# Performance work log

Hardware: AMD Instinct MI355X
Metric: run time of the kernel (lower is better)

Reference implementation:

```python
import jax, jax.numpy as jnp
import numpy as np

C = 64          # residual channels
N_LAYERS = 30
MAX_STEPS = 200
SQRT2 = 2.0 ** 0.5


def _conv1d(x, W, b, dilation=1, pad=0):
    # x: [B, Cin, T], W: [Cout, Cin, K], b: [Cout]
    y = jax.lax.conv_general_dilated(
        x, W, window_strides=(1,), padding=[(pad, pad)],
        rhs_dilation=(dilation,), dimension_numbers=('NCH', 'OIH', 'NCH'))
    return y + b[None, :, None]


def _silu(x):
    return x * jax.nn.sigmoid(x)


def _emb_table():
    steps = jnp.arange(MAX_STEPS, dtype=jnp.float32)[:, None]      # [200,1]
    dims = jnp.arange(64, dtype=jnp.float32)[None, :]              # [1,64]
    t = steps * 10.0 ** (dims * 4.0 / 63.0)                        # [200,64]
    return jnp.concatenate([jnp.sin(t), jnp.cos(t)], axis=1)       # [200,128]


def setup_inputs() -> dict:
    key = jax.random.key(0)
    ks = jax.random.split(key, 20)
    B, T = 4, 16384
    f32 = jnp.float32
    inp = {
        'audio': jax.random.normal(ks[0], (B, 1, T), dtype=f32),
        'diffusion_step': jax.random.randint(ks[1], (B,), 0, MAX_STEPS),
        # input projection Conv1d(1, 64, 1)
        'in_W': jax.random.normal(ks[2], (C, 1, 1), f32) * 1.0,
        'in_b': jax.random.normal(ks[3], (C,), f32) * 0.01,
        # diffusion embedding MLP 128->512->512
        'p1_W': jax.random.normal(ks[4], (512, 128), f32) * (1.0 / np.sqrt(128)),
        'p1_b': jnp.zeros((512,), f32),
        'p2_W': jax.random.normal(ks[5], (512, 512), f32) * (1.0 / np.sqrt(512)),
        'p2_b': jnp.zeros((512,), f32),
        # per-layer params (stacked over 30 layers)
        'dw_W': jax.random.normal(ks[6], (N_LAYERS, 2 * C, C, 3), f32) * (1.0 / np.sqrt(3 * C)),
        'dw_b': jnp.zeros((N_LAYERS, 2 * C), f32),
        'dp_W': jax.random.normal(ks[7], (N_LAYERS, C, 512), f32) * (1.0 / np.sqrt(512)),
        'dp_b': jnp.zeros((N_LAYERS, C), f32),
        'op_W': jax.random.normal(ks[8], (N_LAYERS, 2 * C, C, 1), f32) * (1.0 / np.sqrt(C)),
        'op_b': jnp.zeros((N_LAYERS, 2 * C), f32),
        # skip projection Conv1d(64,64,1)
        'sk_W': jax.random.normal(ks[9], (C, C, 1), f32) * (1.0 / np.sqrt(C)),
        'sk_b': jnp.zeros((C,), f32),
        # output projection Conv1d(64,1,1), weight zero-init like original
        'out_W': jnp.zeros((1, C, 1), f32),
        'out_b': jax.random.normal(ks[10], (1,), f32) * 0.01,
    }
    return inp


def reference(audio, diffusion_step, in_W, in_b, p1_W, p1_b, p2_W, p2_b,
              dw_W, dw_b, dp_W, dp_b, op_W, op_b, sk_W, sk_b, out_W, out_b):
    x = jax.nn.relu(_conv1d(audio, in_W, in_b))                    # [B,64,T]
    # diffusion embedding
    t = _emb_table()[diffusion_step]                               # [B,128]
    t = _silu(t @ p1_W.T + p1_b)                                   # [B,512]
    t = _silu(t @ p2_W.T + p2_b)                                   # [B,512]
    skip = None
    for i in range(N_LAYERS):
        d = 2 ** (i % 10)
        cond = (t @ dp_W[i].T + dp_b[i])[:, :, None]               # [B,64,1]
        y = _conv1d(x + cond, dw_W[i], dw_b[i], dilation=d, pad=d) # [B,128,T]
        gate, filt = y[:, :C], y[:, C:]
        y = jax.nn.sigmoid(gate) * jnp.tanh(filt)                  # [B,64,T]
        y = _conv1d(y, op_W[i], op_b[i])                           # [B,128,T]
        residual, sk = y[:, :C], y[:, C:]
        x = (x + residual) / SQRT2
        skip = sk if skip is None else skip + sk
    x = skip / np.sqrt(float(N_LAYERS)).astype(np.float32)
    x = jax.nn.relu(_conv1d(x, sk_W, sk_b))
    return _conv1d(x, out_W, out_b)                                # [B,1,T]
```

## Files before the change

### kernel.cpp

```cpp
#include <hip/hip_runtime.h>
#include <math.h>

#define C 64
#define NL 30
#define T 16384
#define B 4

typedef __bf16 bf16_t;
typedef __bf16 bf16x8 __attribute__((ext_vector_type(8)));
typedef __bf16 bf16x4 __attribute__((ext_vector_type(4)));
typedef float f32x4 __attribute__((ext_vector_type(4)));

typedef const __attribute__((address_space(1))) unsigned int glb_u32;
typedef __attribute__((address_space(3))) unsigned int lds_u32;

constexpr float INV_SQRT2   = 0.70710678118654752440f;
constexpr float INV_SQRT_NL = 0.18257418583505537115f;

__device__ __forceinline__ float fsig(float x) {
    return __builtin_amdgcn_rcpf(1.f + __builtin_amdgcn_exp2f(-1.44269504089f * x));
}
__device__ __forceinline__ float ftanh(float x) {
    return fmaf(2.f, __builtin_amdgcn_rcpf(1.f + __builtin_amdgcn_exp2f(-2.88539008178f * x)), -1.f);
}
__device__ __forceinline__ int swz(int off) { return off ^ ((off >> 3) & 0x70); }

__global__ void pack_weights(const float* __restrict__ dw_W,
                             const float* __restrict__ op_W,
                             const float* __restrict__ sk_W,
                             bf16_t* __restrict__ convpk,
                             bf16_t* __restrict__ oppk,
                             bf16_t* __restrict__ skpk) {
    int idx = blockIdx.x * 256 + threadIdx.x;
    const int ndw = NL * 128 * 192;
    const int nop = NL * 128 * 64;
    if (idx < ndw) {
        int k = idx % 192; int r = idx / 192;
        int oc = r % 128;  int l = r / 128;
        int tap = k >> 6, ic = k & 63;
        convpk[idx] = (bf16_t)dw_W[((l * 128 + oc) * 64 + ic) * 3 + tap];
    } else if (idx < ndw + nop) {
        oppk[idx - ndw] = (bf16_t)op_W[idx - ndw];
    } else if (idx < ndw + nop + 4096) {
        int j = idx - ndw - nop;
        skpk[j] = (bf16_t)(sk_W[j] * INV_SQRT_NL);
    }
}

__global__ void cond_embp1(const int* __restrict__ step,
                           const float* __restrict__ p1_W, const float* __restrict__ p1_b,
                           float* __restrict__ h1out) {
    __shared__ float e[128];
    __shared__ float red[256];
    int b = blockIdx.x, blk = blockIdx.y, tid = threadIdx.x;
    int s = step[b];
    if (tid < 128) {
        int d = tid & 63;
        float tf = (float)s * powf(10.f, (float)d * 4.f / 63.f);
        double td = (double)tf;
        e[tid] = (tid < 64) ? (float)sin(td) : (float)cos(td);
    }
    __syncthreads();
    int ol = tid >> 2, q = tid & 3;
    int o = blk * 64 + ol;
    const float4* wr = (const float4*)(p1_W + o * 128 + q * 32);
    const float4* ev = (const float4*)(e + q * 32);
    float a = 0.f;
    #pragma unroll
    for (int j = 0; j < 8; ++j) {
        float4 wv = wr[j]; float4 xv = ev[j];
        a = fmaf(wv.x, xv.x, a); a = fmaf(wv.y, xv.y, a);
        a = fmaf(wv.z, xv.z, a); a = fmaf(wv.w, xv.w, a);
    }
    red[tid] = a;
    __syncthreads();
    if (q == 0) {
        float v = red[tid] + red[tid + 1] + red[tid + 2] + red[tid + 3] + p1_b[o];
        h1out[b * 512 + o] = v / (1.f + expf(-v));
    }
}

__global__ void cond_p2(const float* __restrict__ h1,
                        const float* __restrict__ p2_W, const float* __restrict__ p2_b,
                        float* __restrict__ h2out) {
    __shared__ float red[256];
    int b = blockIdx.x, blk = blockIdx.y, tid = threadIdx.x;
    int ol = tid >> 2, q = tid & 3;
    int o = blk * 64 + ol;
    const float4* wr = (const float4*)(p2_W + o * 512 + q * 128);
    const float4* hv = (const float4*)(h1 + b * 512 + q * 128);
    float a = 0.f;
    #pragma unroll 8
    for (int j = 0; j < 32; ++j) {
        float4 wv = wr[j]; float4 xv = hv[j];
        a = fmaf(wv.x, xv.x, a); a = fmaf(wv.y, xv.y, a);
        a = fmaf(wv.z, xv.z, a); a = fmaf(wv.w, xv.w, a);
    }
    red[tid] = a;
    __syncthreads();
    if (q == 0) {
        float v = red[tid] + red[tid + 1] + red[tid + 2] + red[tid + 3] + p2_b[o];
        h2out[b * 512 + o] = v / (1.f + expf(-v));
    }
}

__global__ void cond_stage2(const float* __restrict__ h2,
                            const float* __restrict__ dp_W, const float* __restrict__ dp_b,
                            float* __restrict__ cond) {
    __shared__ float part[256];
    int l = blockIdx.x, b = blockIdx.y;
    int tid = threadIdx.x;
    int o = tid >> 2, q = tid & 3;
    const float4* wr = (const float4*)(dp_W + ((size_t)l * C + o) * 512 + q * 128);
    const float4* h = (const float4*)(h2 + b * 512 + q * 128);
    float a = 0.f;
    #pragma unroll 8
    for (int j = 0; j < 32; ++j) {
        float4 wv = wr[j]; float4 hv = h[j];
        a = fmaf(wv.x, hv.x, a); a = fmaf(wv.y, hv.y, a);
        a = fmaf(wv.z, hv.z, a); a = fmaf(wv.w, hv.w, a);
    }
    part[tid] = a;
    __syncthreads();
    if (q == 0) {
        cond[(l * B + b) * C + o] =
            part[tid] + part[tid + 1] + part[tid + 2] + part[tid + 3] + dp_b[l * C + o];
    }
}

__global__ void cond_fold(const bf16_t* __restrict__ convpk,
                          const float* __restrict__ dw_b,
                          const float* __restrict__ cond,
                          float* __restrict__ bias2) {
    int l = blockIdx.x, b = blockIdx.y;
    int oc = threadIdx.x;
    const bf16_t* wr = convpk + ((size_t)l * 128 + oc) * 192;
    const float* cd = cond + (l * B + b) * C;
    float a = dw_b[l * 128 + oc];
    #pragma unroll 3
    for (int tap = 0; tap < 3; ++tap) {
        #pragma unroll
        for (int ic = 0; ic < 64; ++ic)
            a = fmaf((float)wr[tap * 64 + ic], cd[ic], a);
    }
    bias2[(l * B + b) * 128 + oc] = a;
}

__global__ void in_conv(const float* __restrict__ audio,
                        const float* __restrict__ in_W, const float* __restrict__ in_b,
                        bf16_t* __restrict__ x) {
    int idx = blockIdx.x * 256 + threadIdx.x;
    int cb = idx & 7;
    int t = (idx >> 3) & (T - 1);
    int b = idx >> 17;
    float av = audio[b * T + t];
    bf16x8 o;
    #pragma unroll
    for (int j = 0; j < 8; ++j) {
        int c = cb * 8 + j;
        o[j] = (bf16_t)fmaxf(fmaf(in_W[c], av, in_b[c]), 0.f);
    }
    *(bf16x8*)(x + ((size_t)b * T + t) * 64 + cb * 8) = o;
}

__global__ __launch_bounds__(256) void layer_kernel(
    const bf16_t* __restrict__ x_in, bf16_t* __restrict__ x_out, bf16_t* __restrict__ skip,
    const bf16_t* __restrict__ convpk, const bf16_t* __restrict__ oppk,
    const float* __restrict__ bias2, const float* __restrict__ op_b,
    const bf16_t* __restrict__ zpage,
    int layer, int dil, int first)
{
    __shared__ uint4 smem_u[2048];
    char* sm = (char*)smem_u;

    int tid = threadIdx.x;
    int w = __builtin_amdgcn_readfirstlane(tid >> 6);
    int l = tid & 63;
    int lr = l & 15;
    int g = l >> 4;
    int b = blockIdx.y;
    int tbase = blockIdx.x * 128;
    const bf16_t* xb = x_in + (size_t)b * T * 64;

    bf16x8 cA[2][6];
    const bf16_t* cw = convpk + (size_t)layer * 128 * 192;
    #pragma unroll
    for (int mf = 0; mf < 2; ++mf)
        #pragma unroll
        for (int kf = 0; kf < 6; ++kf)
            cA[mf][kf] = *(const bf16x8*)(cw + (mf * 64 + w * 16 + lr) * 192 + kf * 32 + g * 8);
    bf16x8 oA[2][2];
    const bf16_t* ow = oppk + (size_t)layer * 128 * 64;
    #pragma unroll
    for (int mf = 0; mf < 2; ++mf)
        #pragma unroll
        for (int kf = 0; kf < 2; ++kf)
            oA[mf][kf] = *(const bf16x8*)(ow + (mf * 64 + w * 16 + lr) * 64 + kf * 32 + g * 8);

    f32x4 bC[2], bO[2];
    const float* b2 = bias2 + (layer * B + b) * 128;
    const float* ob = op_b + layer * 2 * C;
    #pragma unroll
    for (int mf = 0; mf < 2; ++mf)
        #pragma unroll
        for (int r = 0; r < 4; ++r) {
            bC[mf][r] = b2[mf * 64 + w * 16 + g * 4 + r];
            bO[mf][r] = ob[mf * 64 + w * 16 + g * 4 + r];
        }

    size_t bb = (size_t)b * T * 64;

    for (int st = 0; st < 2; ++st) {
        int t0 = tbase + st * 64;

        #pragma unroll
        for (int it = 0; it < 6; ++it) {
            int qq = it * 256 + w * 64 + l;
            int slice = qq >> 9;
            int row = (qq >> 3) & 63;
            int c16 = qq & 7;
            int ts = t0 + row + (slice - 1) * dil;
            int c16s = c16 ^ (row & 7);
            const bf16_t* src = ((unsigned)ts < (unsigned)T)
                ? (xb + (size_t)ts * 64 + c16s * 8)
                : (zpage + c16s * 8);
            __builtin_amdgcn_global_load_lds(
                (glb_u32*)src,
                (lds_u32*)(sm + (it * 256 + w * 64) * 16),
                16, 0, 0);
        }
        __syncthreads();

        f32x4 acc[2][4];
        #pragma unroll
        for (int mf = 0; mf < 2; ++mf)
            #pragma unroll
            for (int nf = 0; nf < 4; ++nf) acc[mf][nf] = bC[mf];
        #pragma unroll
        for (int kf = 0; kf < 6; ++kf) {
            int tap = kf >> 1;
            int kc = (kf & 1) * 32;
            bf16x8 Bf[4];
            #pragma unroll
            for (int nf = 0; nf < 4; ++nf) {
                int off = tap * 8192 + (nf * 16 + lr) * 128 + (kc + g * 8) * 2;
                Bf[nf] = *(const bf16x8*)(sm + swz(off));
            }
            #pragma unroll
            for (int mf = 0; mf < 2; ++mf)
                #pragma unroll
                for (int nf = 0; nf < 4; ++nf)
                    acc[mf][nf] = __builtin_amdgcn_mfma_f32_16x16x32_bf16(
                        cA[mf][kf], Bf[nf], acc[mf][nf], 0, 0, 0);
        }

        #pragma unroll
        for (int nf = 0; nf < 4; ++nf) {
            union { bf16_t h[4]; uint2 u; } zp;
            #pragma unroll
            for (int r = 0; r < 4; ++r)
                zp.h[r] = (bf16_t)(fsig(acc[0][nf][r]) * ftanh(acc[1][nf][r]));
            int off = 24576 + (nf * 16 + lr) * 128 + (w * 16 + g * 4) * 2;
            *(uint2*)(sm + swz(off)) = zp.u;
        }
        __syncthreads();

        f32x4 acc2[2][4];
        #pragma unroll
        for (int mf = 0; mf < 2; ++mf)
            #pragma unroll
            for (int nf = 0; nf < 4; ++nf) acc2[mf][nf] = bO[mf];
        #pragma unroll
        for (int kf = 0; kf < 2; ++kf) {
            bf16x8 Zf[4];
            #pragma unroll
            for (int nf = 0; nf < 4; ++nf) {
                int off = 24576 + (nf * 16 + lr) * 128 + (kf * 32 + g * 8) * 2;
                Zf[nf] = *(const bf16x8*)(sm + swz(off));
            }
            #pragma unroll
            for (int mf = 0; mf < 2; ++mf)
                #pragma unroll
                for (int nf = 0; nf < 4; ++nf)
                    acc2[mf][nf] = __builtin_amdgcn_mfma_f32_16x16x32_bf16(
                        oA[mf][kf], Zf[nf], acc2[mf][nf], 0, 0, 0);
        }

        #pragma unroll
        for (int nf = 0; nf < 4; ++nf) {
            int t = t0 + nf * 16 + lr;
            int c0 = w * 16 + g * 4;
            int xoff = 8192 + (nf * 16 + lr) * 128 + c0 * 2;
            bf16x4 xv = *(const bf16x4*)(sm + swz(xoff));
            bf16x4 ro, so;
            bf16_t* sp = skip + bb + (size_t)t * 64 + c0;
            if (first) {
                #pragma unroll
                for (int r = 0; r < 4; ++r) {
                    ro[r] = (bf16_t)(((float)xv[r] + acc2[0][nf][r]) * INV_SQRT2);
                    so[r] = (bf16_t)acc2[1][nf][r];
                }
            } else {
                bf16x4 sv = *(const bf16x4*)sp;
                #pragma unroll
                for (int r = 0; r < 4; ++r) {
                    ro[r] = (bf16_t)(((float)xv[r] + acc2[0][nf][r]) * INV_SQRT2);
                    so[r] = (bf16_t)((float)sv[r] + acc2[1][nf][r]);
                }
            }
            *(bf16x4*)(x_out + bb + (size_t)t * 64 + c0) = ro;
            *(bf16x4*)sp = so;
        }
        if (st == 0) __syncthreads();
    }
}

__global__ __launch_bounds__(256) void final_kernel(
    const bf16_t* __restrict__ skip, const bf16_t* __restrict__ skpk,
    const float* __restrict__ sk_b,
    const float* __restrict__ out_W, const float* __restrict__ out_b,
    float* __restrict__ out)
{
    __shared__ uint4 tile_u[512];
    __shared__ float part[16][66];
    unsigned char* sm = (unsigned char*)tile_u;
    int tid = threadIdx.x;
    int w = __builtin_amdgcn_readfirstlane(tid >> 6);
    int l = tid & 63, lr = l & 15, g = l >> 4;
    int b = blockIdx.y, t0 = blockIdx.x * 64;
    const bf16_t* sb = skip + (size_t)b * T * 64;

    #pragma unroll
    for (int it = 0; it < 2; ++it) {
        int q = it * 256 + tid;
        int row = q >> 3, c16 = q & 7;
        uint4 val = *(const uint4*)(sb + (size_t)(t0 + row) * 64 + c16 * 8);
        *(uint4*)(sm + swz(row * 128 + c16 * 16)) = val;
    }

    bf16x8 aS[2];
    #pragma unroll
    for (int kf = 0; kf < 2; ++kf)
        aS[kf] = *(const bf16x8*)(skpk + (w * 16 + lr) * 64 + kf * 32 + g * 8);
    f32x4 acc[4];
    #pragma unroll
    for (int nf = 0; nf < 4; ++nf)
        #pragma unroll
        for (int r = 0; r < 4; ++r) acc[nf][r] = sk_b[w * 16 + g * 4 + r];
    __syncthreads();

    #pragma unroll
    for (int kf = 0; kf < 2; ++kf) {
        bf16x8 Bf[4];
        #pragma unroll
        for (int nf = 0; nf < 4; ++nf) {
            int off = (nf * 16 + lr) * 128 + (kf * 32 + g * 8) * 2;
            Bf[nf] = *(const bf16x8*)(sm + swz(off));
        }
        #pragma unroll
        for (int nf = 0; nf < 4; ++nf)
            acc[nf] = __builtin_amdgcn_mfma_f32_16x16x32_bf16(aS[kf], Bf[nf], acc[nf], 0, 0, 0);
    }

    #pragma unroll
    for (int nf = 0; nf < 4; ++nf) {
        float o = 0.f;
        #pragma unroll
        for (int r = 0; r < 4; ++r)
            o = fmaf(out_W[w * 16 + g * 4 + r], fmaxf(acc[nf][r], 0.f), o);
        part[w * 4 + g][nf * 16 + lr] = o;
    }
    __syncthreads();
    if (tid < 64) {
        float o = out_b[0];
        #pragma unroll
        for (int j = 0; j < 16; ++j) o += part[j][tid];
        out[(size_t)b * T + t0 + tid] = o;
    }
}

extern "C" void kernel_launch(void* const* d_in, const int* in_sizes, int n_in,
                              void* d_out, int out_size, void* d_ws, size_t ws_size,
                              hipStream_t stream) {
    const float* audio = (const float*)d_in[0];
    const int*   dstep = (const int*)d_in[1];
    const float* in_W  = (const float*)d_in[2];
    const float* in_b  = (const float*)d_in[3];
    const float* p1_W  = (const float*)d_in[4];
    const float* p1_b  = (const float*)d_in[5];
    const float* p2_W  = (const float*)d_in[6];
    const float* p2_b  = (const float*)d_in[7];
    const float* dw_W  = (const float*)d_in[8];
    const float* dw_b  = (const float*)d_in[9];
    const float* dp_W  = (const float*)d_in[10];
    const float* dp_b  = (const float*)d_in[11];
    const float* op_W  = (const float*)d_in[12];
    const float* op_b  = (const float*)d_in[13];
    const float* sk_W  = (const float*)d_in[14];
    const float* sk_b  = (const float*)d_in[15];
    const float* out_W = (const float*)d_in[16];
    const float* out_b = (const float*)d_in[17];

    float* ws = (float*)d_ws;
    const size_t NXE = (size_t)B * T * 64;
    float* cond  = ws;
    float* h1    = cond + NL * B * C;
    float* h2    = h1 + B * 512;
    float* bias2 = h2 + B * 512;
    float* zpg   = bias2 + NL * B * 128;
    bf16_t* xA   = (bf16_t*)(zpg + 128);
    bf16_t* xB   = xA + NXE;
    bf16_t* skip = xB + NXE;
    bf16_t* convpk = skip + NXE;
    bf16_t* oppk   = convpk + (size_t)NL * 128 * 192;
    bf16_t* skpk   = oppk + (size_t)NL * 128 * 64;

    hipMemsetAsync(zpg, 0, 512, stream);
    hipLaunchKernelGGL(pack_weights, dim3(3856), dim3(256), 0, stream,
                       dw_W, op_W, sk_W, convpk, oppk, skpk);
    hipLaunchKernelGGL(cond_embp1, dim3(B, 8), dim3(256), 0, stream,
                       dstep, p1_W, p1_b, h1);
    hipLaunchKernelGGL(cond_p2, dim3(B, 8), dim3(256), 0, stream,
                       h1, p2_W, p2_b, h2);
    hipLaunchKernelGGL(cond_stage2, dim3(NL, B), dim3(256), 0, stream,
                       h2, dp_W, dp_b, cond);
    hipLaunchKernelGGL(cond_fold, dim3(NL, B), dim3(128), 0, stream,
                       convpk, dw_b, cond, bias2);
    hipLaunchKernelGGL(in_conv, dim3(B * T * 8 / 256), dim3(256), 0, stream,
                       audio, in_W, in_b, xA);
    for (int i = 0; i < NL; ++i) {
        bf16_t* xin  = (i & 1) ? xB : xA;
        bf16_t* xout = (i & 1) ? xA : xB;
        int dil = 1 << (i % 10);
        hipLaunchKernelGGL(layer_kernel, dim3(T / 128, B), dim3(256), 0, stream,
                           xin, xout, skip, convpk, oppk, bias2, op_b,
                           (const bf16_t*)zpg, i, dil, (i == 0) ? 1 : 0);
    }
    hipLaunchKernelGGL(final_kernel, dim3(T / 64, B), dim3(256), 0, stream,
                       skip, skpk, sk_b, out_W, out_b, (float*)d_out);
}
```

Measured before the change: 491.3 us.

## Run both time halves concurrently with 512-thread blocks and fuse cond kernels

The layer kernel now uses 512 threads (8 waves), so the two 64-step time sub-tiles that one block previously handled one after the other are processed in parallel by two groups of four waves. All six gather loads are issued up front into a doubled 64KB LDS buffer, removing the serial loop and its extra barriers, and the gather overlaps the weight-fragment loads. Separately, cond_stage2 and cond_fold are merged into one kernel, saving a launch and a global round trip. The larger LDS footprint and block size may limit how many blocks fit on each CU.

```diff
diff --git a/kernel.cpp b/kernel.cpp
--- a/kernel.cpp
+++ b/kernel.cpp
@@ -104,46 +104,43 @@
     }
 }
 
-__global__ void cond_stage2(const float* __restrict__ h2,
-                            const float* __restrict__ dp_W, const float* __restrict__ dp_b,
-                            float* __restrict__ cond) {
-    __shared__ float part[256];
+__global__ void cond_stage2b(const float* __restrict__ h2,
+                             const float* __restrict__ dp_W, const float* __restrict__ dp_b,
+                             const bf16_t* __restrict__ convpk,
+                             const float* __restrict__ dw_b,
+                             float* __restrict__ bias2) {
+    __shared__ float red[256];
+    __shared__ float cond_s[64];
     int l = blockIdx.x, b = blockIdx.y;
     int tid = threadIdx.x;
-    int o = tid >> 2, q = tid & 3;
-    const float4* wr = (const float4*)(dp_W + ((size_t)l * C + o) * 512 + q * 128);
-    const float4* h = (const float4*)(h2 + b * 512 + q * 128);
-    float a = 0.f;
-    #pragma unroll 8
-    for (int j = 0; j < 32; ++j) {
-        float4 wv = wr[j]; float4 hv = h[j];
-        a = fmaf(wv.x, hv.x, a); a = fmaf(wv.y, hv.y, a);
-        a = fmaf(wv.z, hv.z, a); a = fmaf(wv.w, hv.w, a);
-    }
-    part[tid] = a;
-    __syncthreads();
-    if (q == 0) {
-        cond[(l * B + b) * C + o] =
-            part[tid] + part[tid + 1] + part[tid + 2] + part[tid + 3] + dp_b[l * C + o];
-    }
-}
-
-__global__ void cond_fold(const bf16_t* __restrict__ convpk,
-                          const float* __restrict__ dw_b,
-                          const float* __restrict__ cond,
-                          float* __restrict__ bias2) {
-    int l = blockIdx.x, b = blockIdx.y;
-    int oc = threadIdx.x;
-    const bf16_t* wr = convpk + ((size_t)l * 128 + oc) * 192;
-    const float* cd = cond + (l * B + b) * C;
-    float a = dw_b[l * 128 + oc];
-    #pragma unroll 3
-    for (int tap = 0; tap < 3; ++tap) {
-        #pragma unroll
-        for (int ic = 0; ic < 64; ++ic)
-            a = fmaf((float)wr[tap * 64 + ic], cd[ic], a);
-    }
-    bias2[(l * B + b) * 128 + oc] = a;
+    {
+        int o = tid >> 2, q = tid & 3;
+        const float4* wr = (const float4*)(dp_W + ((size_t)l * C + o) * 512 + q * 128);
+        const float4* h = (const float4*)(h2 + b * 512 + q * 128);
+        float a = 0.f;
+        #pragma unroll 8
+        for (int j = 0; j < 32; ++j) {
+            float4 wv = wr[j]; float4 hv = h[j];
+            a = fmaf(wv.x, hv.x, a); a = fmaf(wv.y, hv.y, a);
+            a = fmaf(wv.z, hv.z, a); a = fmaf(wv.w, hv.w, a);
+        }
+        red[tid] = a;
+        __syncthreads();
+        if (q == 0)
+            cond_s[o] = red[tid] + red[tid + 1] + red[tid + 2] + red[tid + 3] + dp_b[l * C + o];
+    }
+    __syncthreads();
+    int oc = tid & 127, kh = tid >> 7;
+    const bf16_t* wr = convpk + ((size_t)l * 128 + oc) * 192 + kh * 96;
+    float a = kh ? 0.f : dw_b[l * 128 + oc];
+    #pragma unroll
+    for (int j = 0; j < 96; ++j)
+        a = fmaf((float)wr[j], cond_s[(kh * 96 + j) & 63], a);
+    __syncthreads();
+    red[tid] = a;
+    __syncthreads();
+    if (tid < 128)
+        bias2[(l * B + b) * 128 + tid] = red[tid] + red[tid + 128];
 }
 
 __global__ void in_conv(const float* __restrict__ audio,
@@ -163,18 +160,20 @@
     *(bf16x8*)(x + ((size_t)b * T + t) * 64 + cb * 8) = o;
 }
 
-__global__ __launch_bounds__(256) void layer_kernel(
+__global__ __launch_bounds__(512, 4) void layer_kernel(
     const bf16_t* __restrict__ x_in, bf16_t* __restrict__ x_out, bf16_t* __restrict__ skip,
     const bf16_t* __restrict__ convpk, const bf16_t* __restrict__ oppk,
     const float* __restrict__ bias2, const float* __restrict__ op_b,
     const bf16_t* __restrict__ zpage,
     int layer, int dil, int first)
 {
-    __shared__ uint4 smem_u[2048];
+    __shared__ uint4 smem_u[4096];
     char* sm = (char*)smem_u;
 
     int tid = threadIdx.x;
-    int w = __builtin_amdgcn_readfirstlane(tid >> 6);
+    int w8 = __builtin_amdgcn_readfirstlane(tid >> 6);
+    int wq = w8 & 3;
+    int h  = w8 >> 2;
     int l = tid & 63;
     int lr = l & 15;
     int g = l >> 4;
@@ -182,136 +181,134 @@
     int tbase = blockIdx.x * 128;
     const bf16_t* xb = x_in + (size_t)b * T * 64;
 
+    #pragma unroll
+    for (int it = 0; it < 6; ++it) {
+        int hh = it / 3;
+        int slice = it % 3;
+        int row = tid >> 3;
+        int c16 = l & 7;
+        int ts = tbase + hh * 64 + row + (slice - 1) * dil;
+        int c16s = c16 ^ (row & 7);
+        const bf16_t* src = ((unsigned)ts < (unsigned)T)
+            ? (xb + (size_t)ts * 64 + c16s * 8)
+            : (zpage + c16s * 8);
+        __builtin_amdgcn_global_load_lds(
+            (glb_u32*)src,
+            (lds_u32*)(sm + it * 8192 + w8 * 1024),
+            16, 0, 0);
+    }
+
     bf16x8 cA[2][6];
     const bf16_t* cw = convpk + (size_t)layer * 128 * 192;
     #pragma unroll
     for (int mf = 0; mf < 2; ++mf)
         #pragma unroll
         for (int kf = 0; kf < 6; ++kf)
-            cA[mf][kf] = *(const bf16x8*)(cw + (mf * 64 + w * 16 + lr) * 192 + kf * 32 + g * 8);
+            cA[mf][kf] = *(const bf16x8*)(cw + (mf * 64 + wq * 16 + lr) * 192 + kf * 32 + g * 8);
+
+    f32x4 acc[2][4];
+    const float* b2 = bias2 + (layer * B + b) * 128;
+    #pragma unroll
+    for (int mf = 0; mf < 2; ++mf) {
+        f32x4 bv;
+        #pragma unroll
+        for (int r = 0; r < 4; ++r) bv[r] = b2[mf * 64 + wq * 16 + g * 4 + r];
+        #pragma unroll
+        for (int nf = 0; nf < 4; ++nf) acc[mf][nf] = bv;
+    }
+    __syncthreads();
+
+    int hbase = h * 24576;
+    #pragma unroll
+    for (int kf = 0; kf < 6; ++kf) {
+        int tap = kf >> 1;
+        int kc = (kf & 1) * 32;
+        bf16x8 Bf[4];
+        #pragma unroll
+        for (int nf = 0; nf < 4; ++nf) {
+            int off = hbase + tap * 8192 + (nf * 16 + lr) * 128 + (kc + g * 8) * 2;
+            Bf[nf] = *(const bf16x8*)(sm + swz(off));
+        }
+        #pragma unroll
+        for (int mf = 0; mf < 2; ++mf)
+            #pragma unroll
+            for (int nf = 0; nf < 4; ++nf)
+                acc[mf][nf] = __builtin_amdgcn_mfma_f32_16x16x32_bf16(
+                    cA[mf][kf], Bf[nf], acc[mf][nf], 0, 0, 0);
+    }
+
     bf16x8 oA[2][2];
     const bf16_t* ow = oppk + (size_t)layer * 128 * 64;
     #pragma unroll
     for (int mf = 0; mf < 2; ++mf)
         #pragma unroll
         for (int kf = 0; kf < 2; ++kf)
-            oA[mf][kf] = *(const bf16x8*)(ow + (mf * 64 + w * 16 + lr) * 64 + kf * 32 + g * 8);
-
-    f32x4 bC[2], bO[2];
-    const float* b2 = bias2 + (layer * B + b) * 128;
+            oA[mf][kf] = *(const bf16x8*)(ow + (mf * 64 + wq * 16 + lr) * 64 + kf * 32 + g * 8);
+
+    int zbase = 49152 + h * 8192;
+    #pragma unroll
+    for (int nf = 0; nf < 4; ++nf) {
+        union { bf16_t hh[4]; uint2 u; } zp;
+        #pragma unroll
+        for (int r = 0; r < 4; ++r)
+            zp.hh[r] = (bf16_t)(fsig(acc[0][nf][r]) * ftanh(acc[1][nf][r]));
+        int off = zbase + (nf * 16 + lr) * 128 + (wq * 16 + g * 4) * 2;
+        *(uint2*)(sm + swz(off)) = zp.u;
+    }
+    __syncthreads();
+
+    f32x4 acc2[2][4];
     const float* ob = op_b + layer * 2 * C;
     #pragma unroll
-    for (int mf = 0; mf < 2; ++mf)
-        #pragma unroll
-        for (int r = 0; r < 4; ++r) {
-            bC[mf][r] = b2[mf * 64 + w * 16 + g * 4 + r];
-            bO[mf][r] = ob[mf * 64 + w * 16 + g * 4 + r];
+    for (int mf = 0; mf < 2; ++mf) {
+        f32x4 bv;
+        #pragma unroll
+        for (int r = 0; r < 4; ++r) bv[r] = ob[mf * 64 + wq * 16 + g * 4 + r];
+        #pragma unroll
+        for (int nf = 0; nf < 4; ++nf) acc2[mf][nf] = bv;
+    }
+    #pragma unroll
+    for (int kf = 0; kf < 2; ++kf) {
+        bf16x8 Zf[4];
+        #pragma unroll
+        for (int nf = 0; nf < 4; ++nf) {
+            int off = zbase + (nf * 16 + lr) * 128 + (kf * 32 + g * 8) * 2;
+            Zf[nf] = *(const bf16x8*)(sm + swz(off));
         }
-
-    size_t bb = (size_t)b * T * 64;
-
-    for (int st = 0; st < 2; ++st) {
-        int t0 = tbase + st * 64;
-
-        #pragma unroll
-        for (int it = 0; it < 6; ++it) {
-            int qq = it * 256 + w * 64 + l;
-            int slice = qq >> 9;
-            int row = (qq >> 3) & 63;
-            int c16 = qq & 7;
-            int ts = t0 + row + (slice - 1) * dil;
-            int c16s = c16 ^ (row & 7);
-            const bf16_t* src = ((unsigned)ts < (unsigned)T)
-                ? (xb + (size_t)ts * 64 + c16s * 8)
-                : (zpage + c16s * 8);
-            __builtin_amdgcn_global_load_lds(
-                (glb_u32*)src,
-                (lds_u32*)(sm + (it * 256 + w * 64) * 16),
-                16, 0, 0);
-        }
-        __syncthreads();
-
-        f32x4 acc[2][4];
         #pragma unroll
         for (int mf = 0; mf < 2; ++mf)
             #pragma unroll
-            for (int nf = 0; nf < 4; ++nf) acc[mf][nf] = bC[mf];
-        #pragma unroll
-        for (int kf = 0; kf < 6; ++kf) {
-            int tap = kf >> 1;
-            int kc = (kf & 1) * 32;
-            bf16x8 Bf[4];
+            for (int nf = 0; nf < 4; ++nf)
+                acc2[mf][nf] = __builtin_amdgcn_mfma_f32_16x16x32_bf16(
+                    oA[mf][kf], Zf[nf], acc2[mf][nf], 0, 0, 0);
+    }
+
+    size_t bb = (size_t)b * T * 64;
+    int t0 = tbase + h * 64;
+    #pragma unroll
+    for (int nf = 0; nf < 4; ++nf) {
+        int t = t0 + nf * 16 + lr;
+        int c0 = wq * 16 + g * 4;
+        int xoff = hbase + 8192 + (nf * 16 + lr) * 128 + c0 * 2;
+        bf16x4 xv = *(const bf16x4*)(sm + swz(xoff));
+        bf16x4 ro, so;
+        bf16_t* sp = skip + bb + (size_t)t * 64 + c0;
+        if (first) {
             #pragma unroll
-            for (int nf = 0; nf < 4; ++nf) {
-                int off = tap * 8192 + (nf * 16 + lr) * 128 + (kc + g * 8) * 2;
-                Bf[nf] = *(const bf16x8*)(sm + swz(off));
+            for (int r = 0; r < 4; ++r) {
+                ro[r] = (bf16_t)(((float)xv[r] + acc2[0][nf][r]) * INV_SQRT2);
+                so[r] = (bf16_t)acc2[1][nf][r];
             }
+        } else {
+            bf16x4 sv = *(const bf16x4*)sp;
             #pragma unroll
-            for (int mf = 0; mf < 2; ++mf)
-                #pragma unroll
-                for (int nf = 0; nf < 4; ++nf)
-                    acc[mf][nf] = __builtin_amdgcn_mfma_f32_16x16x32_bf16(
-                        cA[mf][kf], Bf[nf], acc[mf][nf], 0, 0, 0);
+            for (int r = 0; r < 4; ++r) {
+                ro[r] = (bf16_t)(((float)xv[r] + acc2[0][nf][r]) * INV_SQRT2);
+                so[r] = (bf16_t)((float)sv[r] + acc2[1][nf][r]);
+            }
         }
-
-        #pragma unroll
-        for (int nf = 0; nf < 4; ++nf) {
-            union { bf16_t h[4]; uint2 u; } zp;
-            #pragma unroll
-            for (int r = 0; r < 4; ++r)
-                zp.h[r] = (bf16_t)(fsig(acc[0][nf][r]) * ftanh(acc[1][nf][r]));
-            int off = 24576 + (nf * 16 + lr) * 128 + (w * 16 + g * 4) * 2;
-            *(uint2*)(sm + swz(off)) = zp.u;
-        }
-        __syncthreads();
-
-        f32x4 acc2[2][4];
-        #pragma unroll
-        for (int mf = 0; mf < 2; ++mf)
-            #pragma unroll
-            for (int nf = 0; nf < 4; ++nf) acc2[mf][nf] = bO[mf];
-        #pragma unroll
-        for (int kf = 0; kf < 2; ++kf) {
-            bf16x8 Zf[4];
-            #pragma unroll
-            for (int nf = 0; nf < 4; ++nf) {
-                int off = 24576 + (nf * 16 + lr) * 128 + (kf * 32 + g * 8) * 2;
-                Zf[nf] = *(const bf16x8*)(sm + swz(off));
-            }
-            #pragma unroll
-            for (int mf = 0; mf < 2; ++mf)
-                #pragma unroll
-                for (int nf = 0; nf < 4; ++nf)
-                    acc2[mf][nf] = __builtin_amdgcn_mfma_f32_16x16x32_bf16(
-                        oA[mf][kf], Zf[nf], acc2[mf][nf], 0, 0, 0);
-        }
-
-        #pragma unroll
-        for (int nf = 0; nf < 4; ++nf) {
-            int t = t0 + nf * 16 + lr;
-            int c0 = w * 16 + g * 4;
-            int xoff = 8192 + (nf * 16 + lr) * 128 + c0 * 2;
-            bf16x4 xv = *(const bf16x4*)(sm + swz(xoff));
-            bf16x4 ro, so;
-            bf16_t* sp = skip + bb + (size_t)t * 64 + c0;
-            if (first) {
-                #pragma unroll
-                for (int r = 0; r < 4; ++r) {
-                    ro[r] = (bf16_t)(((float)xv[r] + acc2[0][nf][r]) * INV_SQRT2);
-                    so[r] = (bf16_t)acc2[1][nf][r];
-                }
-            } else {
-                bf16x4 sv = *(const bf16x4*)sp;
-                #pragma unroll
-                for (int r = 0; r < 4; ++r) {
-                    ro[r] = (bf16_t)(((float)xv[r] + acc2[0][nf][r]) * INV_SQRT2);
-                    so[r] = (bf16_t)((float)sv[r] + acc2[1][nf][r]);
-                }
-            }
-            *(bf16x4*)(x_out + bb + (size_t)t * 64 + c0) = ro;
-            *(bf16x4*)sp = so;
-        }
-        if (st == 0) __syncthreads();
+        *(bf16x4*)(x_out + bb + (size_t)t * 64 + c0) = ro;
+        *(bf16x4*)sp = so;
     }
 }
 
@@ -403,8 +400,7 @@
 
     float* ws = (float*)d_ws;
     const size_t NXE = (size_t)B * T * 64;
-    float* cond  = ws;
-    float* h1    = cond + NL * B * C;
+    float* h1    = ws;
     float* h2    = h1 + B * 512;
     float* bias2 = h2 + B * 512;
     float* zpg   = bias2 + NL * B * 128;
@@ -422,17 +418,15 @@
                        dstep, p1_W, p1_b, h1);
     hipLaunchKernelGGL(cond_p2, dim3(B, 8), dim3(256), 0, stream,
                        h1, p2_W, p2_b, h2);
-    hipLaunchKernelGGL(cond_stage2, dim3(NL, B), dim3(256), 0, stream,
-                       h2, dp_W, dp_b, cond);
-    hipLaunchKernelGGL(cond_fold, dim3(NL, B), dim3(128), 0, stream,
-                       convpk, dw_b, cond, bias2);
+    hipLaunchKernelGGL(cond_stage2b, dim3(NL, B), dim3(256), 0, stream,
+                       h2, dp_W, dp_b, convpk, dw_b, bias2);
     hipLaunchKernelGGL(in_conv, dim3(B * T * 8 / 256), dim3(256), 0, stream,
                        audio, in_W, in_b, xA);
     for (int i = 0; i < NL; ++i) {
         bf16_t* xin  = (i & 1) ? xB : xA;
         bf16_t* xout = (i & 1) ? xA : xB;
         int dil = 1 << (i % 10);
-        hipLaunchKernelGGL(layer_kernel, dim3(T / 128, B), dim3(256), 0, stream,
+        hipLaunchKernelGGL(layer_kernel, dim3(T / 128, B), dim3(512), 0, stream,
                            xin, xout, skip, convpk, oppk, bias2, op_b,
                            (const bf16_t*)zpg, i, dil, (i == 0) ? 1 : 0);
     }
```

After: 544.5 us. 1.11x slower.
